# Optimization experiments

Measured on AMD Instinct MI355X. Metric: run time of the kernel, lower is better.

Reference implementation:

```python
import jax, jax.numpy as jnp
import numpy as np

T = 2048          # tokens (single-sequence prefill)
HID = 4096        # hidden_size
NH = 32           # num attention heads
NKV = 8           # num kv heads (GQA)
HD = 128          # head_dim
QKV_OUT = (NH + 2 * NKV) * HD  # 6144
THETA = 10000.0
SCALING = HD ** -0.5


def setup_inputs() -> dict:
    key = jax.random.key(0)
    ks = jax.random.split(key, 8)
    positions = jnp.arange(T, dtype=jnp.int32)
    # per-token int8 quantized hidden states (symmetric, [-127,127])
    q_act = jax.random.randint(ks[0], (T, HID), -127, 128, dtype=jnp.int32)
    # per-token dynamic activation scale
    act_scale = jax.random.uniform(ks[1], (T,), jnp.float32) * 0.01 + 0.001
    # int4 weights stored unsigned [0,15] with per-output-channel scale & zero point
    w_qkv_q = jax.random.randint(ks[2], (QKV_OUT, HID), 0, 16, dtype=jnp.int32)
    w_qkv_scale = jax.random.uniform(ks[3], (QKV_OUT,), jnp.float32) * 0.01 + 0.001
    w_qkv_zero = jax.random.uniform(ks[4], (QKV_OUT,), jnp.float32) * 2.0 + 7.0
    w_o_q = jax.random.randint(ks[5], (HID, HID), 0, 16, dtype=jnp.int32)
    w_o_scale = jax.random.uniform(ks[6], (HID,), jnp.float32) * 0.01 + 0.001
    w_o_zero = jax.random.uniform(ks[7], (HID,), jnp.float32) * 2.0 + 7.0
    return dict(positions=positions, q_act=q_act, act_scale=act_scale,
                w_qkv_q=w_qkv_q, w_qkv_scale=w_qkv_scale, w_qkv_zero=w_qkv_zero,
                w_o_q=w_o_q, w_o_scale=w_o_scale, w_o_zero=w_o_zero)


def w4a8_linear(qa_f, s_a, a_sum, qw, s_w, z_w):
    # y[t,o] = s_a[t]*s_w[o] * ( (qa @ qw^T)[t,o] - z_w[o]*sum_j qa[t,j] )
    acc = jnp.matmul(qa_f, qw.astype(jnp.float32).T)  # [T, O]
    return (s_a[:, None] * s_w[None, :]) * (acc - z_w[None, :] * a_sum[:, None])


def apply_rope(x, positions):
    # neox-style RoPE over full head_dim
    half = HD // 2
    inv_freq = THETA ** (-jnp.arange(0, half, dtype=jnp.float32) / half * 1.0)
    inv_freq = 1.0 / (THETA ** (jnp.arange(0, HD, 2, dtype=jnp.float32) / HD))
    freqs = positions.astype(jnp.float32)[:, None] * inv_freq[None, :]  # [T, HD/2]
    cos = jnp.cos(freqs)[:, None, :]
    sin = jnp.sin(freqs)[:, None, :]
    x1, x2 = x[..., :half], x[..., half:]
    return jnp.concatenate([x1 * cos - x2 * sin, x2 * cos + x1 * sin], axis=-1)


def dynamic_quant_with_sum(x):
    # per-token symmetric int8 dynamic quantization + fused sum
    s = jnp.maximum(jnp.max(jnp.abs(x), axis=-1), 1e-8) / 127.0  # [T]
    q = jnp.clip(jnp.round(x / s[:, None]), -127, 127)
    return q, s, jnp.sum(q, axis=-1)


def reference(positions, q_act, act_scale, w_qkv_q, w_qkv_scale, w_qkv_zero,
              w_o_q, w_o_scale, w_o_zero):
    qa_f = q_act.astype(jnp.float32)
    a_sum = jnp.sum(qa_f, axis=-1)  # fused activation sum
    qkv = w4a8_linear(qa_f, act_scale, a_sum, w_qkv_q, w_qkv_scale, w_qkv_zero)
    q, k, v = jnp.split(qkv, [NH * HD, NH * HD + NKV * HD], axis=-1)
    q = q.reshape(T, NH, HD)
    k = k.reshape(T, NKV, HD)
    v = v.reshape(T, NKV, HD)
    q = apply_rope(q, positions)
    k = apply_rope(k, positions)
    # GQA: repeat kv heads
    rep = NH // NKV
    k = jnp.repeat(k, rep, axis=1)  # [T, NH, HD]
    v = jnp.repeat(v, rep, axis=1)
    scores = jnp.einsum('qhd,khd->hqk', q, k) * SCALING  # [NH, T, T]
    causal = jnp.tril(jnp.ones((T, T), dtype=bool))
    scores = jnp.where(causal[None], scores, -jnp.inf)
    probs = jax.nn.softmax(scores, axis=-1)
    attn = jnp.einsum('hqk,khd->qhd', probs, v).reshape(T, NH * HD)
    # invoke_quant_fuse_sum: dynamic per-token quantization of attn output
    q2, s2, sum2 = dynamic_quant_with_sum(attn)
    out = w4a8_linear(q2, s2, sum2, w_o_q, w_o_scale, w_o_zero)
    return out
```

## Files before the change

kernel.cpp:

```cpp
#include <hip/hip_runtime.h>

#define T 2048
#define HID 4096
#define NH 32
#define NKV 8
#define HD 128
#define QKV_OUT ((NH + 2*NKV) * HD)
#define SCALING 0.08838834764831843f

typedef __attribute__((ext_vector_type(8))) short bfrag;
typedef __attribute__((ext_vector_type(4))) float ffrag;
typedef __attribute__((ext_vector_type(4))) int  ifrag;
typedef __attribute__((ext_vector_type(16))) char c16;

__device__ __forceinline__ short f2bf(float f) {
  unsigned u = __builtin_bit_cast(unsigned, f);
  u += 0x7fffu + ((u >> 16) & 1u);
  return (short)(u >> 16);
}

__device__ __forceinline__ void split2(float x, short& hi, short& lo) {
  unsigned u = __builtin_bit_cast(unsigned, x);
  unsigned uh = u + (0x7fffu + ((u >> 16) & 1u));
  hi = (short)(uh >> 16);
  float fh = __builtin_bit_cast(float, uh & 0xffff0000u);
  float r = x - fh;
  unsigned ur = __builtin_bit_cast(unsigned, r);
  ur += 0x7fffu + ((ur >> 16) & 1u);
  lo = (short)(ur >> 16);
}

__device__ __forceinline__ void gload_lds16(const void* g, void* l) {
  __builtin_amdgcn_global_load_lds(
      (const __attribute__((address_space(1))) unsigned int*)g,
      (__attribute__((address_space(3))) unsigned int*)l, 16, 0, 0);
}

__global__ __launch_bounds__(256)
void asum_conv(const int* __restrict__ qact, float* __restrict__ a_sum,
               char* __restrict__ a_i8) {
  __shared__ int red[256];
  const int t = blockIdx.x, tid = threadIdx.x;
  const int* row = qact + (size_t)t * HID + tid * 16;
  int s = 0;
  c16 o;
#pragma unroll
  for (int i = 0; i < 4; i++) {
    int4 v = *(const int4*)(row + i * 4);
    s += v.x + v.y + v.z + v.w;
    o[i*4+0] = (char)v.x; o[i*4+1] = (char)v.y;
    o[i*4+2] = (char)v.z; o[i*4+3] = (char)v.w;
  }
  *(c16*)(a_i8 + (size_t)t * HID + tid * 16) = o;
  red[tid] = s; __syncthreads();
  for (int off = 128; off > 0; off >>= 1) {
    if (tid < off) red[tid] += red[tid + off];
    __syncthreads();
  }
  if (tid == 0) a_sum[t] = (float)red[0];
}

__global__ __launch_bounds__(256)
void conv_i2c(const int* __restrict__ src, char* __restrict__ dst, int n16) {
  int idx = blockIdx.x * 256 + threadIdx.x;
  if (idx >= n16) return;
  const int4* s4 = (const int4*)src + (size_t)idx * 4;
  c16 o;
#pragma unroll
  for (int j = 0; j < 4; j++) {
    int4 v = s4[j];
    o[j*4+0] = (char)v.x; o[j*4+1] = (char)v.y;
    o[j*4+2] = (char)v.z; o[j*4+3] = (char)v.w;
  }
  *(c16*)(dst + (size_t)idx * 16) = o;
}

template<bool WI8>
__global__ __launch_bounds__(256)
void gemm_i8(const char* __restrict__ A, const void* __restrict__ Wv,
             const float* __restrict__ s_a, const float* __restrict__ asum,
             const float* __restrict__ s_w, const float* __restrict__ z_w,
             float* __restrict__ C, int M, int N, int K) {
  __shared__ __align__(16) char As[128 * 64];
  __shared__ __align__(16) char Bs[128 * 64];
  const int tid = threadIdx.x;
  const int lane = tid & 63;
  const int quad = lane >> 4, l15 = lane & 15;
  const int wave = tid >> 6;
  const int wm = (wave >> 1) * 64, wn = (wave & 1) * 64;
  const int bm = blockIdx.y * 128, bn = blockIdx.x * 128;
  const int sr = tid >> 2, sc = (tid & 3) * 16;

  ifrag acc[4][4];
#pragma unroll
  for (int mi = 0; mi < 4; mi++)
#pragma unroll
    for (int ni = 0; ni < 4; ni++)
      acc[mi][ni] = (ifrag){0, 0, 0, 0};

  for (int k0 = 0; k0 < K; k0 += 64) {
#pragma unroll
    for (int it = 0; it < 2; it++)
      gload_lds16(A + (size_t)(bm + it * 64 + sr) * K + k0 + sc,
                  &As[it * 4096 + wave * 1024]);
    if constexpr (WI8) {
      const char* W = (const char*)Wv;
#pragma unroll
      for (int it = 0; it < 2; it++)
        gload_lds16(W + (size_t)(bn + it * 64 + sr) * K + k0 + sc,
                    &Bs[it * 4096 + wave * 1024]);
    } else {
      const int* W = (const int*)Wv;
      int r = tid >> 1, hh = (tid & 1) * 32;
#pragma unroll
      for (int i = 0; i < 2; i++) {
        c16 o;
#pragma unroll
        for (int j = 0; j < 4; j++) {
          int4 v = *(const int4*)(W + (size_t)(bn + r) * K + k0 + hh + i * 16 + j * 4);
          o[j*4+0] = (char)v.x; o[j*4+1] = (char)v.y;
          o[j*4+2] = (char)v.z; o[j*4+3] = (char)v.w;
        }
        *(c16*)&Bs[r * 64 + hh + i * 16] = o;
      }
    }
    __syncthreads();

    ifrag af[4], bfv[4];
#pragma unroll
    for (int mi = 0; mi < 4; mi++)
      af[mi] = *(const ifrag*)&As[(wm + mi * 16 + l15) * 64 + quad * 16];
#pragma unroll
    for (int ni = 0; ni < 4; ni++)
      bfv[ni] = *(const ifrag*)&Bs[(wn + ni * 16 + l15) * 64 + quad * 16];
#pragma unroll
    for (int mi = 0; mi < 4; mi++)
#pragma unroll
      for (int ni = 0; ni < 4; ni++)
        acc[mi][ni] = __builtin_amdgcn_mfma_i32_16x16x64_i8(
            af[mi], bfv[ni], acc[mi][ni], 0, 0, 0);
    __syncthreads();
  }

#pragma unroll
  for (int mi = 0; mi < 4; mi++) {
    int row0 = bm + wm + mi * 16 + quad * 4;
#pragma unroll
    for (int r = 0; r < 4; r++) {
      int row = row0 + r;
      float sa = s_a[row], av = asum[row];
#pragma unroll
      for (int ni = 0; ni < 4; ni++) {
        int col = bn + wn + ni * 16 + l15;
        C[(size_t)row * N + col] = (sa * s_w[col]) * ((float)acc[mi][ni][r] - z_w[col] * av);
      }
    }
  }
}

__global__ __launch_bounds__(64)
void rope_kernel(float* __restrict__ qkv, const int* __restrict__ positions) {
  const int b = blockIdx.x;
  const int t = b / (NH + NKV);
  const int h = b % (NH + NKV);
  float* base = qkv + (size_t)t * QKV_OUT + (size_t)h * HD;
  const int i = threadIdx.x;
  float inv = exp2f(-0.20762050593046014f * (float)i);
  float f = (float)positions[t] * inv;
  float s, c;
  sincosf(f, &s, &c);
  float x1 = base[i], x2 = base[i + 64];
  base[i]      = x1 * c - x2 * s;
  base[i + 64] = x2 * c + x1 * s;
}

__global__ __launch_bounds__(256)
void split_kv(const float* __restrict__ qkv,
              short* __restrict__ Kh, short* __restrict__ Kl,
              short* __restrict__ Vth) {
  __shared__ __align__(16) short Vh_lds[128 * 72];
  const int kvh = blockIdx.y;
  const int t0 = blockIdx.x * 64;
  const int tid = threadIdx.x;
#pragma unroll
  for (int i = 0; i < 8; i++) {
    int c = tid + 256 * i;
    int key = c >> 5, dc = c & 31;
    float4 f = *(const float4*)(qkv + (size_t)(t0 + key) * QKV_OUT
                                + (size_t)NH * HD + (size_t)kvh * HD + dc * 4);
    short4 h4, l4;
    split2(f.x, h4.x, l4.x); split2(f.y, h4.y, l4.y);
    split2(f.z, h4.z, l4.z); split2(f.w, h4.w, l4.w);
    size_t o = (size_t)kvh * T * HD + (size_t)(t0 + key) * HD + dc * 4;
    *(short4*)(Kh + o) = h4;
    *(short4*)(Kl + o) = l4;
  }
#pragma unroll
  for (int i = 0; i < 8; i++) {
    int c = tid + 256 * i;
    int key = c >> 5, dc = c & 31;
    float4 f = *(const float4*)(qkv + (size_t)(t0 + key) * QKV_OUT
                                + (size_t)(NH + NKV) * HD + (size_t)kvh * HD + dc * 4);
    Vh_lds[(dc*4+0)*72 + key] = f2bf(f.x);
    Vh_lds[(dc*4+1)*72 + key] = f2bf(f.y);
    Vh_lds[(dc*4+2)*72 + key] = f2bf(f.z);
    Vh_lds[(dc*4+3)*72 + key] = f2bf(f.w);
  }
  __syncthreads();
#pragma unroll
  for (int i = 0; i < 2; i++) {
    int c = tid + 256 * i;
    int row = c >> 2, cc = c & 3;
    size_t o = (size_t)kvh * HD * T + (size_t)row * T + t0 + cc * 8;
    *(bfrag*)(Vth + o) = *(const bfrag*)&Vh_lds[row * 72 + cc * 8];
  }
#pragma unroll
  for (int i = 0; i < 2; i++) {
    int c = tid + 256 * i;
    int row = c >> 2, cc = c & 3;
    size_t o = (size_t)kvh * HD * T + (size_t)row * T + t0 + 32 + cc * 8;
    *(bfrag*)(Vth + o) = *(const bfrag*)&Vh_lds[row * 72 + 32 + cc * 8];
  }
}

__global__ __launch_bounds__(256)
void attn_kernel(const float* __restrict__ qkv,
                 const short* __restrict__ Kh, const short* __restrict__ Kl,
                 const short* __restrict__ Vth,
                 float* __restrict__ attn) {
  __shared__ __align__(16) short Ksh[32 * 136];
  __shared__ __align__(16) short Ksl[32 * 136];
  __shared__ __align__(16) short Vsh[128 * 40];
  __shared__ __align__(16) short Psh[4 * 16 * 40];

  const int kvh = blockIdx.y;
  const int pair = blockIdx.x;
  const int tid = threadIdx.x;
  const int lane = tid & 63;
  const int wv = tid >> 6;
  const int l15 = lane & 15, quad = lane >> 4;
  const int h = kvh * 4 + wv;
  short* Pw = Psh + wv * 16 * 40;

  const short* KhB = Kh + (size_t)kvh * T * HD;
  const short* KlB = Kl + (size_t)kvh * T * HD;
  const short* VhB = Vth + (size_t)kvh * HD * T;

  const int kr = tid >> 4, kc8 = (tid & 15) * 8;
  const int vd = tid >> 2, vc8 = (tid & 3) * 8;

  bfrag rkh0, rkh1, rkl0, rkl1, rv0, rv1;
  auto preload = [&](int k0) {
    rkh0 = *(const bfrag*)(KhB + (size_t)(k0 + kr) * HD + kc8);
    rkh1 = *(const bfrag*)(KhB + (size_t)(k0 + kr + 16) * HD + kc8);
    rkl0 = *(const bfrag*)(KlB + (size_t)(k0 + kr) * HD + kc8);
    rkl1 = *(const bfrag*)(KlB + (size_t)(k0 + kr + 16) * HD + kc8);
    rv0  = *(const bfrag*)(VhB + (size_t)vd * T + k0 + vc8);
    rv1  = *(const bfrag*)(VhB + (size_t)(vd + 64) * T + k0 + vc8);
  };
  preload(0);

  bfrag ones;
#pragma unroll
  for (int j = 0; j < 8; j++) ones[j] = (short)0x3f80;

  for (int pass = 0; pass < 2; pass++) {
    const int qt = pass ? pair : 127 - pair;
    const int q0 = qt * 16;
    const int nk = (q0 >> 5) + 1;

    bfrag qh[4], ql[4];
    const float* qrow = qkv + (size_t)(q0 + l15) * QKV_OUT + (size_t)h * HD;
#pragma unroll
    for (int kc = 0; kc < 4; kc++) {
      float4 f0 = *(const float4*)(qrow + kc * 32 + quad * 8);
      float4 f1 = *(const float4*)(qrow + kc * 32 + quad * 8 + 4);
      float fv[8] = {f0.x, f0.y, f0.z, f0.w, f1.x, f1.y, f1.z, f1.w};
#pragma unroll
      for (int j = 0; j < 8; j++) {
        short hi, lo; split2(fv[j], hi, lo);
        qh[kc][j] = hi; ql[kc][j] = lo;
      }
    }

    ffrag o[8], ol;
    ol = (ffrag){0.f, 0.f, 0.f, 0.f};
#pragma unroll
    for (int n = 0; n < 8; n++) o[n] = (ffrag){0.f, 0.f, 0.f, 0.f};
    float m_i[4] = {-1e30f, -1e30f, -1e30f, -1e30f};

    for (int kt = 0; kt < nk; kt++) {
      const int k0 = kt << 5;
      __syncthreads();
      *(bfrag*)&Ksh[kr * 136 + kc8] = rkh0;
      *(bfrag*)&Ksh[(kr + 16) * 136 + kc8] = rkh1;
      *(bfrag*)&Ksl[kr * 136 + kc8] = rkl0;
      *(bfrag*)&Ksl[(kr + 16) * 136 + kc8] = rkl1;
      *(bfrag*)&Vsh[vd * 40 + vc8] = rv0;
      *(bfrag*)&Vsh[(vd + 64) * 40 + vc8] = rv1;
      if (kt + 1 < nk) preload(k0 + 32);
      else if (pass == 0) preload(0);
      __syncthreads();

      ffrag s[2];
      s[0] = (ffrag){0.f,0.f,0.f,0.f}; s[1] = (ffrag){0.f,0.f,0.f,0.f};
#pragma unroll
      for (int n = 0; n < 2; n++) {
#pragma unroll
        for (int kc = 0; kc < 4; kc++) {
          bfrag bh = *(const bfrag*)&Ksh[(n*16 + l15) * 136 + kc*32 + quad*8];
          bfrag bl = *(const bfrag*)&Ksl[(n*16 + l15) * 136 + kc*32 + quad*8];
          s[n] = __builtin_amdgcn_mfma_f32_16x16x32_bf16(qh[kc], bh, s[n], 0,0,0);
          s[n] = __builtin_amdgcn_mfma_f32_16x16x32_bf16(qh[kc], bl, s[n], 0,0,0);
          s[n] = __builtin_amdgcn_mfma_f32_16x16x32_bf16(ql[kc], bh, s[n], 0,0,0);
        }
      }
      const bool last = (kt == nk - 1);
      float sv[2][4];
#pragma unroll
      for (int n = 0; n < 2; n++)
#pragma unroll
        for (int r = 0; r < 4; r++) {
          float v = s[n][r] * SCALING;
          if (last) {
            int key = k0 + n * 16 + l15;
            int row = q0 + quad * 4 + r;
            if (key > row) v = -1e30f;
          }
          sv[n][r] = v;
        }
      float alpha[4];
#pragma unroll
      for (int r = 0; r < 4; r++) {
        float mt = fmaxf(sv[0][r], sv[1][r]);
        mt = fmaxf(mt, __shfl_xor(mt, 1));
        mt = fmaxf(mt, __shfl_xor(mt, 2));
        mt = fmaxf(mt, __shfl_xor(mt, 4));
        mt = fmaxf(mt, __shfl_xor(mt, 8));
        float m_new = fmaxf(m_i[r], mt);
        alpha[r] = __expf(m_i[r] - m_new);
        m_i[r] = m_new;
      }
#pragma unroll
      for (int n = 0; n < 2; n++)
#pragma unroll
        for (int r = 0; r < 4; r++) {
          float p = __expf(sv[n][r] - m_i[r]);
          Pw[(quad*4 + r) * 40 + n*16 + l15] = f2bf(p);
        }
#pragma unroll
      for (int r = 0; r < 4; r++) ol[r] *= alpha[r];
#pragma unroll
      for (int n = 0; n < 8; n++)
#pragma unroll
        for (int r = 0; r < 4; r++) o[n][r] *= alpha[r];
      bfrag ph = *(const bfrag*)&Pw[l15 * 40 + quad * 8];
      ol = __builtin_amdgcn_mfma_f32_16x16x32_bf16(ph, ones, ol, 0,0,0);
#pragma unroll
      for (int n = 0; n < 8; n++) {
        bfrag vh = *(const bfrag*)&Vsh[(n*16 + l15) * 40 + quad * 8];
        o[n] = __builtin_amdgcn_mfma_f32_16x16x32_bf16(ph, vh, o[n], 0,0,0);
      }
    }

    float inv[4];
#pragma unroll
    for (int r = 0; r < 4; r++) inv[r] = 1.f / ol[r];
#pragma unroll
    for (int n = 0; n < 8; n++)
#pragma unroll
      for (int r = 0; r < 4; r++) {
        int row = q0 + quad * 4 + r;
        attn[(size_t)row * HID + (size_t)h * HD + n * 16 + l15] = o[n][r] * inv[r];
      }
  }
}

__global__ __launch_bounds__(256)
void quant_kernel(const float* __restrict__ x, char* __restrict__ q2,
                  float* __restrict__ s2, float* __restrict__ sum2) {
  __shared__ float red[256];
  const int t = blockIdx.x, tid = threadIdx.x;
  const float* row = x + (size_t)t * HID;
  float4 v[4];
  float m = 0.f;
#pragma unroll
  for (int i = 0; i < 4; i++) {
    v[i] = *(const float4*)(row + tid * 16 + i * 4);
    m = fmaxf(m, fmaxf(fmaxf(fabsf(v[i].x), fabsf(v[i].y)),
                       fmaxf(fabsf(v[i].z), fabsf(v[i].w))));
  }
  red[tid] = m; __syncthreads();
  for (int off = 128; off > 0; off >>= 1) {
    if (tid < off) red[tid] = fmaxf(red[tid], red[tid + off]);
    __syncthreads();
  }
  float s = fmaxf(red[0], 1e-8f) / 127.f;
  __syncthreads();
  float ssum = 0.f;
  c16 o;
#pragma unroll
  for (int i = 0; i < 4; i++) {
    float q;
    q = fminf(127.f, fmaxf(-127.f, rintf(v[i].x / s))); ssum += q; o[i*4+0] = (char)(int)q;
    q = fminf(127.f, fmaxf(-127.f, rintf(v[i].y / s))); ssum += q; o[i*4+1] = (char)(int)q;
    q = fminf(127.f, fmaxf(-127.f, rintf(v[i].z / s))); ssum += q; o[i*4+2] = (char)(int)q;
    q = fminf(127.f, fmaxf(-127.f, rintf(v[i].w / s))); ssum += q; o[i*4+3] = (char)(int)q;
  }
  *(c16*)(q2 + (size_t)t * HID + tid * 16) = o;
  red[tid] = ssum; __syncthreads();
  for (int off = 128; off > 0; off >>= 1) {
    if (tid < off) red[tid] += red[tid + off];
    __syncthreads();
  }
  if (tid == 0) { s2[t] = s; sum2[t] = red[0]; }
}

extern "C" void kernel_launch(void* const* d_in, const int* in_sizes, int n_in,
                              void* d_out, int out_size, void* d_ws, size_t ws_size,
                              hipStream_t stream) {
  const int*   positions   = (const int*)d_in[0];
  const int*   q_act       = (const int*)d_in[1];
  const float* act_scale   = (const float*)d_in[2];
  const int*   w_qkv_q     = (const int*)d_in[3];
  const float* w_qkv_scale = (const float*)d_in[4];
  const float* w_qkv_zero  = (const float*)d_in[5];
  const int*   w_o_q       = (const int*)d_in[6];
  const float* w_o_scale   = (const float*)d_in[7];
  const float* w_o_zero    = (const float*)d_in[8];
  float* out = (float*)d_out;

  size_t off = 0;
  auto alloc = [&](size_t bytes) -> void* {
    void* p = (char*)d_ws + off;
    off += (bytes + 255) & ~(size_t)255;
    return p;
  };
  float* qkv   = (float*)alloc((size_t)T * QKV_OUT * 4);
  char*  a_i8  = (char*)alloc((size_t)T * HID);
  char*  q2    = (char*)alloc((size_t)T * HID);
  short* Kh    = (short*)alloc((size_t)NKV * T * HD * 2);
  short* Kl    = (short*)alloc((size_t)NKV * T * HD * 2);
  short* Vth   = (short*)alloc((size_t)NKV * T * HD * 2);
  float* a_sum = (float*)alloc(T * 4);
  float* s2    = (float*)alloc(T * 4);
  float* sum2  = (float*)alloc(T * 4);
  char* wqkv_i8 = (char*)alloc((size_t)QKV_OUT * HID);
  char* wo_i8   = (char*)alloc((size_t)HID * HID);
  const bool wconv = (ws_size >= off);

  asum_conv<<<T, 256, 0, stream>>>(q_act, a_sum, a_i8);
  if (wconv) {
    conv_i2c<<<(QKV_OUT * HID / 16 + 255) / 256, 256, 0, stream>>>(w_qkv_q, wqkv_i8, QKV_OUT * HID / 16);
    conv_i2c<<<(HID * HID / 16 + 255) / 256, 256, 0, stream>>>(w_o_q, wo_i8, HID * HID / 16);
    gemm_i8<true><<<dim3(QKV_OUT / 128, T / 128), 256, 0, stream>>>(
        a_i8, wqkv_i8, act_scale, a_sum, w_qkv_scale, w_qkv_zero, qkv, T, QKV_OUT, HID);
  } else {
    gemm_i8<false><<<dim3(QKV_OUT / 128, T / 128), 256, 0, stream>>>(
        a_i8, w_qkv_q, act_scale, a_sum, w_qkv_scale, w_qkv_zero, qkv, T, QKV_OUT, HID);
  }
  rope_kernel<<<T * (NH + NKV), 64, 0, stream>>>(qkv, positions);
  split_kv<<<dim3(T / 64, NKV), 256, 0, stream>>>(qkv, Kh, Kl, Vth);
  attn_kernel<<<dim3(64, NKV), 256, 0, stream>>>(qkv, Kh, Kl, Vth, out);
  quant_kernel<<<T, 256, 0, stream>>>(out, q2, s2, sum2);
  if (wconv) {
    gemm_i8<true><<<dim3(HID / 128, T / 128), 256, 0, stream>>>(
        q2, wo_i8, s2, sum2, w_o_scale, w_o_zero, out, T, HID, HID);
  } else {
    gemm_i8<false><<<dim3(HID / 128, T / 128), 256, 0, stream>>>(
        q2, w_o_q, s2, sum2, w_o_scale, w_o_zero, out, T, HID, HID);
  }
}
```

Before: 564.7 us.

## Fuse RoPE into K split and attention Q load, one q-tile per block

Removes the standalone RoPE kernel: K rotation now happens inside split_kv and Q rotation inside the attention kernel when Q is loaded, so the qkv buffer no longer takes an extra read-modify-write pass and one launch goes away. The attention grid doubles to one 16-row query tile per block, heaviest first, instead of pairing two tiles per block. It also skips the rescaling of the output accumulators when no row max changed. In exchange, sincos is recomputed per head inside attention, and load balance now depends on the hardware scheduler.

Result: slower. 680.3 us (+20.5%).

```diff
diff --git a/kernel.cpp b/kernel.cpp
--- a/kernel.cpp
+++ b/kernel.cpp
@@ -7,6 +7,7 @@
 #define HD 128
 #define QKV_OUT ((NH + 2*NKV) * HD)
 #define SCALING 0.08838834764831843f
+#define ROPE_C 0.20762050593046014f
 
 typedef __attribute__((ext_vector_type(8))) short bfrag;
 typedef __attribute__((ext_vector_type(4))) float ffrag;
@@ -158,24 +159,8 @@
   }
 }
 
-__global__ __launch_bounds__(64)
-void rope_kernel(float* __restrict__ qkv, const int* __restrict__ positions) {
-  const int b = blockIdx.x;
-  const int t = b / (NH + NKV);
-  const int h = b % (NH + NKV);
-  float* base = qkv + (size_t)t * QKV_OUT + (size_t)h * HD;
-  const int i = threadIdx.x;
-  float inv = exp2f(-0.20762050593046014f * (float)i);
-  float f = (float)positions[t] * inv;
-  float s, c;
-  sincosf(f, &s, &c);
-  float x1 = base[i], x2 = base[i + 64];
-  base[i]      = x1 * c - x2 * s;
-  base[i + 64] = x2 * c + x1 * s;
-}
-
-__global__ __launch_bounds__(256)
-void split_kv(const float* __restrict__ qkv,
+__global__ __launch_bounds__(256)
+void split_kv(const float* __restrict__ qkv, const int* __restrict__ positions,
               short* __restrict__ Kh, short* __restrict__ Kl,
               short* __restrict__ Vth) {
   __shared__ __align__(16) short Vh_lds[128 * 72];
@@ -183,17 +168,31 @@
   const int t0 = blockIdx.x * 64;
   const int tid = threadIdx.x;
 #pragma unroll
-  for (int i = 0; i < 8; i++) {
-    int c = tid + 256 * i;
-    int key = c >> 5, dc = c & 31;
-    float4 f = *(const float4*)(qkv + (size_t)(t0 + key) * QKV_OUT
-                                + (size_t)NH * HD + (size_t)kvh * HD + dc * 4);
-    short4 h4, l4;
-    split2(f.x, h4.x, l4.x); split2(f.y, h4.y, l4.y);
-    split2(f.z, h4.z, l4.z); split2(f.w, h4.w, l4.w);
-    size_t o = (size_t)kvh * T * HD + (size_t)(t0 + key) * HD + dc * 4;
-    *(short4*)(Kh + o) = h4;
-    *(short4*)(Kl + o) = l4;
+  for (int it = 0; it < 4; it++) {
+    int c = tid + 256 * it;
+    int key = c >> 4, dc = c & 15;
+    const float* kr = qkv + (size_t)(t0 + key) * QKV_OUT
+                      + (size_t)NH * HD + (size_t)kvh * HD;
+    float4 a = *(const float4*)(kr + dc * 4);
+    float4 b = *(const float4*)(kr + dc * 4 + 64);
+    float av[4] = {a.x, a.y, a.z, a.w};
+    float bv[4] = {b.x, b.y, b.z, b.w};
+    float pos = (float)positions[t0 + key];
+    short4 ha, la, hb, lb;
+    short hh, ll;
+#pragma unroll
+    for (int jj = 0; jj < 4; jj++) {
+      float fr = pos * exp2f(-ROPE_C * (float)(dc * 4 + jj));
+      float sn, cs; sincosf(fr, &sn, &cs);
+      float x1 = av[jj], x2 = bv[jj];
+      float r1 = x1 * cs - x2 * sn;
+      float r2 = x2 * cs + x1 * sn;
+      split2(r1, hh, ll); ((short*)&ha)[jj] = hh; ((short*)&la)[jj] = ll;
+      split2(r2, hh, ll); ((short*)&hb)[jj] = hh; ((short*)&lb)[jj] = ll;
+    }
+    size_t o1 = (size_t)kvh * T * HD + (size_t)(t0 + key) * HD + dc * 4;
+    *(short4*)(Kh + o1) = ha;      *(short4*)(Kl + o1) = la;
+    *(short4*)(Kh + o1 + 64) = hb; *(short4*)(Kl + o1 + 64) = lb;
   }
 #pragma unroll
   for (int i = 0; i < 8; i++) {
@@ -224,7 +223,7 @@
 }
 
 __global__ __launch_bounds__(256)
-void attn_kernel(const float* __restrict__ qkv,
+void attn_kernel(const float* __restrict__ qkv, const int* __restrict__ positions,
                  const short* __restrict__ Kh, const short* __restrict__ Kl,
                  const short* __restrict__ Vth,
                  float* __restrict__ attn) {
@@ -234,13 +233,15 @@
   __shared__ __align__(16) short Psh[4 * 16 * 40];
 
   const int kvh = blockIdx.y;
-  const int pair = blockIdx.x;
+  const int qt = gridDim.x - 1 - blockIdx.x;
+  const int q0 = qt * 16;
   const int tid = threadIdx.x;
   const int lane = tid & 63;
   const int wv = tid >> 6;
   const int l15 = lane & 15, quad = lane >> 4;
   const int h = kvh * 4 + wv;
   short* Pw = Psh + wv * 16 * 40;
+  const int nk = (q0 >> 5) + 1;
 
   const short* KhB = Kh + (size_t)kvh * T * HD;
   const short* KlB = Kl + (size_t)kvh * T * HD;
@@ -260,120 +261,136 @@
   };
   preload(0);
 
-  bfrag ones;
-#pragma unroll
-  for (int j = 0; j < 8; j++) ones[j] = (short)0x3f80;
-
-  for (int pass = 0; pass < 2; pass++) {
-    const int qt = pass ? pair : 127 - pair;
-    const int q0 = qt * 16;
-    const int nk = (q0 >> 5) + 1;
-
-    bfrag qh[4], ql[4];
-    const float* qrow = qkv + (size_t)(q0 + l15) * QKV_OUT + (size_t)h * HD;
+  const int trow = q0 + l15;
+  float fv[4][8];
+  {
+    const float* qrow = qkv + (size_t)trow * QKV_OUT + (size_t)h * HD;
 #pragma unroll
     for (int kc = 0; kc < 4; kc++) {
       float4 f0 = *(const float4*)(qrow + kc * 32 + quad * 8);
       float4 f1 = *(const float4*)(qrow + kc * 32 + quad * 8 + 4);
-      float fv[8] = {f0.x, f0.y, f0.z, f0.w, f1.x, f1.y, f1.z, f1.w};
+      fv[kc][0]=f0.x; fv[kc][1]=f0.y; fv[kc][2]=f0.z; fv[kc][3]=f0.w;
+      fv[kc][4]=f1.x; fv[kc][5]=f1.y; fv[kc][6]=f1.z; fv[kc][7]=f1.w;
+    }
+    float pos = (float)positions[trow];
+#pragma unroll
+    for (int kc = 0; kc < 2; kc++)
 #pragma unroll
       for (int j = 0; j < 8; j++) {
-        short hi, lo; split2(fv[j], hi, lo);
-        qh[kc][j] = hi; ql[kc][j] = lo;
-      }
-    }
-
-    ffrag o[8], ol;
-    ol = (ffrag){0.f, 0.f, 0.f, 0.f};
-#pragma unroll
-    for (int n = 0; n < 8; n++) o[n] = (ffrag){0.f, 0.f, 0.f, 0.f};
-    float m_i[4] = {-1e30f, -1e30f, -1e30f, -1e30f};
-
-    for (int kt = 0; kt < nk; kt++) {
-      const int k0 = kt << 5;
-      __syncthreads();
-      *(bfrag*)&Ksh[kr * 136 + kc8] = rkh0;
-      *(bfrag*)&Ksh[(kr + 16) * 136 + kc8] = rkh1;
-      *(bfrag*)&Ksl[kr * 136 + kc8] = rkl0;
-      *(bfrag*)&Ksl[(kr + 16) * 136 + kc8] = rkl1;
-      *(bfrag*)&Vsh[vd * 40 + vc8] = rv0;
-      *(bfrag*)&Vsh[(vd + 64) * 40 + vc8] = rv1;
-      if (kt + 1 < nk) preload(k0 + 32);
-      else if (pass == 0) preload(0);
-      __syncthreads();
-
-      ffrag s[2];
-      s[0] = (ffrag){0.f,0.f,0.f,0.f}; s[1] = (ffrag){0.f,0.f,0.f,0.f};
-#pragma unroll
-      for (int n = 0; n < 2; n++) {
-#pragma unroll
-        for (int kc = 0; kc < 4; kc++) {
-          bfrag bh = *(const bfrag*)&Ksh[(n*16 + l15) * 136 + kc*32 + quad*8];
-          bfrag bl = *(const bfrag*)&Ksl[(n*16 + l15) * 136 + kc*32 + quad*8];
-          s[n] = __builtin_amdgcn_mfma_f32_16x16x32_bf16(qh[kc], bh, s[n], 0,0,0);
-          s[n] = __builtin_amdgcn_mfma_f32_16x16x32_bf16(qh[kc], bl, s[n], 0,0,0);
-          s[n] = __builtin_amdgcn_mfma_f32_16x16x32_bf16(ql[kc], bh, s[n], 0,0,0);
+        int i = kc * 32 + quad * 8 + j;
+        float fr = pos * exp2f(-ROPE_C * (float)i);
+        float sn, cs; sincosf(fr, &sn, &cs);
+        float x1 = fv[kc][j], x2 = fv[kc + 2][j];
+        fv[kc][j]     = x1 * cs - x2 * sn;
+        fv[kc + 2][j] = x2 * cs + x1 * sn;
+      }
+  }
+  bfrag qh[4], ql[4];
+#pragma unroll
+  for (int kc = 0; kc < 4; kc++)
+#pragma unroll
+    for (int j = 0; j < 8; j++) {
+      short hi, lo; split2(fv[kc][j], hi, lo);
+      qh[kc][j] = hi; ql[kc][j] = lo;
+    }
+
+  bfrag ones;
+#pragma unroll
+  for (int j = 0; j < 8; j++) ones[j] = (short)0x3f80;
+
+  ffrag o[8], ol;
+  ol = (ffrag){0.f, 0.f, 0.f, 0.f};
+#pragma unroll
+  for (int n = 0; n < 8; n++) o[n] = (ffrag){0.f, 0.f, 0.f, 0.f};
+  float m_i[4] = {-1e30f, -1e30f, -1e30f, -1e30f};
+
+  for (int kt = 0; kt < nk; kt++) {
+    const int k0 = kt << 5;
+    __syncthreads();
+    *(bfrag*)&Ksh[kr * 136 + kc8] = rkh0;
+    *(bfrag*)&Ksh[(kr + 16) * 136 + kc8] = rkh1;
+    *(bfrag*)&Ksl[kr * 136 + kc8] = rkl0;
+    *(bfrag*)&Ksl[(kr + 16) * 136 + kc8] = rkl1;
+    *(bfrag*)&Vsh[vd * 40 + vc8] = rv0;
+    *(bfrag*)&Vsh[(vd + 64) * 40 + vc8] = rv1;
+    if (kt + 1 < nk) preload(k0 + 32);
+    __syncthreads();
+
+    ffrag s[2];
+    s[0] = (ffrag){0.f,0.f,0.f,0.f}; s[1] = (ffrag){0.f,0.f,0.f,0.f};
+#pragma unroll
+    for (int n = 0; n < 2; n++) {
+#pragma unroll
+      for (int kc = 0; kc < 4; kc++) {
+        bfrag bh = *(const bfrag*)&Ksh[(n*16 + l15) * 136 + kc*32 + quad*8];
+        bfrag bl = *(const bfrag*)&Ksl[(n*16 + l15) * 136 + kc*32 + quad*8];
+        s[n] = __builtin_amdgcn_mfma_f32_16x16x32_bf16(qh[kc], bh, s[n], 0,0,0);
+        s[n] = __builtin_amdgcn_mfma_f32_16x16x32_bf16(qh[kc], bl, s[n], 0,0,0);
+        s[n] = __builtin_amdgcn_mfma_f32_16x16x32_bf16(ql[kc], bh, s[n], 0,0,0);
+      }
+    }
+    const bool last = (kt == nk - 1);
+    float sv[2][4];
+#pragma unroll
+    for (int n = 0; n < 2; n++)
+#pragma unroll
+      for (int r = 0; r < 4; r++) {
+        float v = s[n][r] * SCALING;
+        if (last) {
+          int key = k0 + n * 16 + l15;
+          int row = q0 + quad * 4 + r;
+          if (key > row) v = -1e30f;
         }
-      }
-      const bool last = (kt == nk - 1);
-      float sv[2][4];
-#pragma unroll
-      for (int n = 0; n < 2; n++)
-#pragma unroll
-        for (int r = 0; r < 4; r++) {
-          float v = s[n][r] * SCALING;
-          if (last) {
-            int key = k0 + n * 16 + l15;
-            int row = q0 + quad * 4 + r;
-            if (key > row) v = -1e30f;
-          }
-          sv[n][r] = v;
-        }
-      float alpha[4];
+        sv[n][r] = v;
+      }
+    float alpha[4];
+    bool anyup = false;
+#pragma unroll
+    for (int r = 0; r < 4; r++) {
+      float mt = fmaxf(sv[0][r], sv[1][r]);
+      mt = fmaxf(mt, __shfl_xor(mt, 1));
+      mt = fmaxf(mt, __shfl_xor(mt, 2));
+      mt = fmaxf(mt, __shfl_xor(mt, 4));
+      mt = fmaxf(mt, __shfl_xor(mt, 8));
+      float m_new = fmaxf(m_i[r], mt);
+      alpha[r] = __expf(m_i[r] - m_new);
+      if (m_new > m_i[r]) anyup = true;
+      m_i[r] = m_new;
+    }
+#pragma unroll
+    for (int n = 0; n < 2; n++)
 #pragma unroll
       for (int r = 0; r < 4; r++) {
-        float mt = fmaxf(sv[0][r], sv[1][r]);
-        mt = fmaxf(mt, __shfl_xor(mt, 1));
-        mt = fmaxf(mt, __shfl_xor(mt, 2));
-        mt = fmaxf(mt, __shfl_xor(mt, 4));
-        mt = fmaxf(mt, __shfl_xor(mt, 8));
-        float m_new = fmaxf(m_i[r], mt);
-        alpha[r] = __expf(m_i[r] - m_new);
-        m_i[r] = m_new;
-      }
-#pragma unroll
-      for (int n = 0; n < 2; n++)
-#pragma unroll
-        for (int r = 0; r < 4; r++) {
-          float p = __expf(sv[n][r] - m_i[r]);
-          Pw[(quad*4 + r) * 40 + n*16 + l15] = f2bf(p);
-        }
+        float p = __expf(sv[n][r] - m_i[r]);
+        Pw[(quad*4 + r) * 40 + n*16 + l15] = f2bf(p);
+      }
+    if (__any(anyup)) {
 #pragma unroll
       for (int r = 0; r < 4; r++) ol[r] *= alpha[r];
 #pragma unroll
       for (int n = 0; n < 8; n++)
 #pragma unroll
         for (int r = 0; r < 4; r++) o[n][r] *= alpha[r];
-      bfrag ph = *(const bfrag*)&Pw[l15 * 40 + quad * 8];
-      ol = __builtin_amdgcn_mfma_f32_16x16x32_bf16(ph, ones, ol, 0,0,0);
-#pragma unroll
-      for (int n = 0; n < 8; n++) {
-        bfrag vh = *(const bfrag*)&Vsh[(n*16 + l15) * 40 + quad * 8];
-        o[n] = __builtin_amdgcn_mfma_f32_16x16x32_bf16(ph, vh, o[n], 0,0,0);
-      }
-    }
-
-    float inv[4];
-#pragma unroll
-    for (int r = 0; r < 4; r++) inv[r] = 1.f / ol[r];
-#pragma unroll
-    for (int n = 0; n < 8; n++)
-#pragma unroll
-      for (int r = 0; r < 4; r++) {
-        int row = q0 + quad * 4 + r;
-        attn[(size_t)row * HID + (size_t)h * HD + n * 16 + l15] = o[n][r] * inv[r];
-      }
-  }
+    }
+    bfrag ph = *(const bfrag*)&Pw[l15 * 40 + quad * 8];
+    ol = __builtin_amdgcn_mfma_f32_16x16x32_bf16(ph, ones, ol, 0,0,0);
+#pragma unroll
+    for (int n = 0; n < 8; n++) {
+      bfrag vh = *(const bfrag*)&Vsh[(n*16 + l15) * 40 + quad * 8];
+      o[n] = __builtin_amdgcn_mfma_f32_16x16x32_bf16(ph, vh, o[n], 0,0,0);
+    }
+  }
+
+  float inv[4];
+#pragma unroll
+  for (int r = 0; r < 4; r++) inv[r] = 1.f / ol[r];
+#pragma unroll
+  for (int n = 0; n < 8; n++)
+#pragma unroll
+    for (int r = 0; r < 4; r++) {
+      int row = q0 + quad * 4 + r;
+      attn[(size_t)row * HID + (size_t)h * HD + n * 16 + l15] = o[n][r] * inv[r];
+    }
 }
 
 __global__ __launch_bounds__(256)
@@ -459,9 +476,8 @@
     gemm_i8<false><<<dim3(QKV_OUT / 128, T / 128), 256, 0, stream>>>(
         a_i8, w_qkv_q, act_scale, a_sum, w_qkv_scale, w_qkv_zero, qkv, T, QKV_OUT, HID);
   }
-  rope_kernel<<<T * (NH + NKV), 64, 0, stream>>>(qkv, positions);
-  split_kv<<<dim3(T / 64, NKV), 256, 0, stream>>>(qkv, Kh, Kl, Vth);
-  attn_kernel<<<dim3(64, NKV), 256, 0, stream>>>(qkv, Kh, Kl, Vth, out);
+  split_kv<<<dim3(T / 64, NKV), 256, 0, stream>>>(qkv, positions, Kh, Kl, Vth);
+  attn_kernel<<<dim3(128, NKV), 256, 0, stream>>>(qkv, positions, Kh, Kl, Vth, out);
   quant_kernel<<<T, 256, 0, stream>>>(out, q2, s2, sum2);
   if (wconv) {
     gemm_i8<true><<<dim3(HID / 128, T / 128), 256, 0, stream>>>(
```
